# Kernel optimization log

Hardware: AMD Instinct MI355X
Metric: run time of the kernel (lower is better)

## Reference

```python
import jax, jax.numpy as jnp
import numpy as np

N = 50000   # nodes
E = 400000  # edges
G = 256     # graphs in batch
D = 256     # out_dim (scalar channel width)
VD = 16     # vector channel width after v_emb


def setup_inputs() -> dict:
    key = jax.random.key(0)
    ks = jax.random.split(key, 12)

    def rn(k, shape, scale=0.02):
        return (jax.random.normal(k, shape) * scale).astype(jnp.float32)

    return dict(
        node_s=jax.random.normal(ks[0], (N, 23), jnp.float32),
        node_v=jax.random.normal(ks[1], (N, 4, 3), jnp.float32),
        edge_s=jax.random.normal(ks[2], (E, 17), jnp.float32),
        edge_index=jax.random.randint(ks[3], (2, E), 0, N, jnp.int32),
        batch=jnp.sort(jax.random.randint(ks[4], (N,), 0, G, jnp.int32)),
        Ws=rn(ks[5], (23, D)), bs=jnp.zeros((D,), jnp.float32),
        Wv=rn(ks[6], (4, VD)), bv=jnp.zeros((VD,), jnp.float32),
        We=rn(ks[7], (18, D)), be=jnp.zeros((D,), jnp.float32),
        Wm1=rn(ks[8], (2 * D + VD + D, D)), bm1=jnp.zeros((D,), jnp.float32),
        Wm2=rn(ks[9], (D, D)), bm2=jnp.zeros((D,), jnp.float32),
        Wn=rn(ks[10], (D + VD, D)), bn=jnp.zeros((D,), jnp.float32),
        gamma=jnp.ones((D,), jnp.float32), beta=jnp.zeros((D,), jnp.float32),
    )


def reference(node_s, node_v, edge_s, edge_index, batch,
              Ws, bs, Wv, bv, We, be, Wm1, bm1, Wm2, bm2, Wn, bn, gamma, beta):
    # --- embeddings ---
    s = node_s @ Ws + bs                                            # [N, D]
    e_in = jnp.concatenate([edge_s, jnp.zeros((edge_s.shape[0], 1), edge_s.dtype)], axis=-1)  # no edge_v branch
    e = e_in @ We + be                                              # [E, D]
    # v_emb: Linear over the 4 vector channels -> [N, VD, 3]
    v = jnp.einsum('nkc,ko->noc', node_v, Wv) + bv[None, :, None]
    v_norm = jnp.linalg.norm(v, axis=-1)                            # [N, VD]

    # --- SimpleGVPConv: gather -> 2-layer MLP per edge -> scatter-mean ---
    src, dst = edge_index[0], edge_index[1]                         # PyG: s_j = s[src], s_i = s[dst]
    m_in = jnp.concatenate([s[dst], s[src], v_norm[src], e], axis=-1)  # [E, 2D+VD+D]
    m = jax.nn.relu(m_in @ Wm1 + bm1) @ Wm2 + bm2                   # [E, D]
    agg = jax.ops.segment_sum(m, dst, num_segments=N)               # [N, D]
    cnt = jax.ops.segment_sum(jnp.ones((E,), m.dtype), dst, num_segments=N)
    s = s + agg / jnp.maximum(cnt, 1.0)[:, None]                    # mean aggr + residual update

    # --- node MLP: Linear -> LayerNorm -> ReLU (dropout = eval identity) ---
    feat = jnp.concatenate([s, v_norm], axis=-1)                    # [N, D+VD]
    h = feat @ Wn + bn                                              # [N, D]
    mu = h.mean(axis=-1, keepdims=True)
    var = h.var(axis=-1, keepdims=True)
    h = (h - mu) * jax.lax.rsqrt(var + 1e-5) * gamma + beta
    h = jax.nn.relu(h)

    # --- global mean pool ---
    gsum = jax.ops.segment_sum(h, batch, num_segments=G)            # [G, D]
    gcnt = jax.ops.segment_sum(jnp.ones((h.shape[0],), h.dtype), batch, num_segments=G)
    return gsum / jnp.maximum(gcnt, 1.0)[:, None]
```

## Files before the change

### kernel.cpp

```cpp
#include <hip/hip_runtime.h>
#include <hip/hip_bf16.h>

typedef unsigned short u16;
typedef __attribute__((ext_vector_type(8))) short short8;
typedef __attribute__((ext_vector_type(4))) short short4v;
typedef __attribute__((ext_vector_type(4))) float f32x4;

#define NN 50000
#define EE 400000
#define GG 256
#define MP 50048
#define KS 64
#define K2 320

static __device__ __forceinline__ __hip_bfloat16 f2b(float x) { return __float2bfloat16(x); }
static __device__ __forceinline__ float u16tof(u16 v) {
    unsigned x = ((unsigned)v) << 16;
    float f;
    __builtin_memcpy(&f, &x, 4);
    return f;
}
static __device__ __forceinline__ u16 ftou16(float x) {
    __hip_bfloat16 h = __float2bfloat16(x);
    u16 b;
    __builtin_memcpy(&b, &h, 2);
    return b;
}
static __device__ __forceinline__ float rlf(float v, int l) {
    unsigned u;
    __builtin_memcpy(&u, &v, 4);
    unsigned r = (unsigned)__builtin_amdgcn_readlane((int)u, l);
    float f;
    __builtin_memcpy(&f, &r, 4);
    return f;
}

static __device__ __forceinline__ float dot256(const float* __restrict__ a,
                                               const float* __restrict__ b, int c) {
    const float* __restrict__ bp = b + c;
    float s0 = 0.f, s1 = 0.f, s2 = 0.f, s3 = 0.f;
    float s4 = 0.f, s5 = 0.f, s6 = 0.f, s7 = 0.f;
#pragma unroll 4
    for (int j = 0; j < 256; j += 8) {
        s0 += a[j]     * bp[(size_t)(j)     * 256];
        s1 += a[j + 1] * bp[(size_t)(j + 1) * 256];
        s2 += a[j + 2] * bp[(size_t)(j + 2) * 256];
        s3 += a[j + 3] * bp[(size_t)(j + 3) * 256];
        s4 += a[j + 4] * bp[(size_t)(j + 4) * 256];
        s5 += a[j + 5] * bp[(size_t)(j + 5) * 256];
        s6 += a[j + 6] * bp[(size_t)(j + 6) * 256];
        s7 += a[j + 7] * bp[(size_t)(j + 7) * 256];
    }
    return ((s0 + s1) + (s2 + s3)) + ((s4 + s5) + (s6 + s7));
}

__global__ __launch_bounds__(256) void phase1(const float* __restrict__ Wm1,
                                              const float* __restrict__ Wn,
                                              const float* __restrict__ Wm2,
                                              const float* __restrict__ We,
                                              const float* __restrict__ be,
                                              const float* __restrict__ bm1,
                                              const float* __restrict__ bm2,
                                              const float* __restrict__ Ws,
                                              const float* __restrict__ bs,
                                              __hip_bfloat16* __restrict__ W1pqT,
                                              __hip_bfloat16* __restrict__ W2T,
                                              float* __restrict__ Wc, float* __restrict__ bc,
                                              float* __restrict__ crow,
                                              const float* __restrict__ node_s,
                                              const float* __restrict__ node_v,
                                              const float* __restrict__ Wv,
                                              const float* __restrict__ bv,
                                              __hip_bfloat16* __restrict__ XL2,
                                              const int* __restrict__ ei,
                                              const int* __restrict__ batch,
                                              int* __restrict__ cnt,
                                              int* __restrict__ gstart) {
    int blk = blockIdx.x, tid = threadIdx.x;
    if (blk < 64) {
        int k = blk;
#pragma unroll
        for (int half = 0; half < 2; ++half) {
            int c = half * 256 + tid;
            int cc = c & 255;
            const float* Wm1h = (c < 256) ? Wm1 : (Wm1 + 256 * 256);
            float v = 0.f;
            if (k < 23) v = dot256(&Ws[k * 256], Wm1h, cc);
            else if (k < 39) { if (c >= 256) v = Wm1[(512 + (k - 23)) * 256 + cc]; }
            else if (k == 39) v = dot256(bs, Wm1h, cc);
            W1pqT[c * KS + k] = f2b(v);
        }
    } else if (blk < 384) {
        int k = blk - 64, c = tid;
        float v = 0.f;
        if (k < 23) v = dot256(&Ws[k * 256], Wn, c);
        else if (k < 39) v = Wn[(256 + (k - 23)) * 256 + c];
        else if (k == 39) v = dot256(bs, Wn, c);
        else if (k < 296) v = dot256(&Wm2[(k - 40) * 256], Wn, c);
        W2T[c * K2 + k] = f2b(v);
    } else if (blk < 403) {
        int b = blk - 384, c = tid;
        if (b < 17) Wc[b * 256 + c] = dot256(&We[b * 256], &Wm1[528 * 256], c);
        else if (b == 17) bc[c] = bm1[c] + dot256(be, &Wm1[528 * 256], c);
        else crow[c] = dot256(bm2, Wn, c);
    } else if (blk < 12903) {
        int w = tid >> 6, lane = tid & 63;
        int n = (blk - 403) * 4 + w;
        if (n < NN) {
            float lv = (lane < 23) ? node_s[(size_t)n * 23 + lane] : 0.f;
            float vv = (lane < 12) ? node_v[(size_t)n * 12 + lane] : 0.f;
            float nvk[12];
#pragma unroll
            for (int k = 0; k < 12; ++k) nvk[k] = __shfl(vv, k, 64);
            float vn = 0.f;
            if (lane < 16) {
                float b0 = bv[lane];
                float vx = b0, vy = b0, vz = b0;
#pragma unroll
                for (int k = 0; k < 4; ++k) {
                    float wv = Wv[k * 16 + lane];
                    vx += nvk[k * 3 + 0] * wv;
                    vy += nvk[k * 3 + 1] * wv;
                    vz += nvk[k * 3 + 2] * wv;
                }
                vn = sqrtf(vx * vx + vy * vy + vz * vz);
            }
            int vsrc = (lane >= 23 && lane < 39) ? (lane - 23) : 0;
            float vbc = __shfl(vn, vsrc, 64);
            float outv;
            if (lane < 23) outv = lv;
            else if (lane < 39) outv = vbc;
            else if (lane == 39) outv = 1.f;
            else outv = 0.f;
            __hip_bfloat16* row = XL2 + (size_t)n * K2;
            row[lane] = f2b(outv);
            if (lane < 24) row[296 + lane] = f2b(0.f);
        }
    } else if (blk < 14466) {
        int e = (blk - 12903) * 256 + tid;
        if (e < EE) atomicAdd(&cnt[ei[EE + e]], 1);
    } else {
        int n = (blk - 14466) * 256 + tid;
        if (n < NN) {
            int bn = batch[n];
            int bp = (n == 0) ? -1 : batch[n - 1];
            for (int g = bp + 1; g <= bn; ++g) gstart[g] = n;
            if (n == NN - 1)
                for (int g = bn + 1; g <= GG; ++g) gstart[g] = NN;
        }
    }
}

__global__ __launch_bounds__(256) void scan1(const int* __restrict__ cnt, int* __restrict__ rowptr,
                                             int* __restrict__ bsum) {
    int tid = threadIdx.x, i = blockIdx.x * 256 + tid;
    __shared__ int sd[256];
    int v = (i < NN) ? cnt[i] : 0;
    sd[tid] = v;
    __syncthreads();
    for (int off = 1; off < 256; off <<= 1) {
        int t = (tid >= off) ? sd[tid - off] : 0;
        __syncthreads();
        sd[tid] += t;
        __syncthreads();
    }
    if (i < NN) rowptr[i] = sd[tid] - v;
    if (tid == 255) bsum[blockIdx.x] = sd[255];
}
__global__ __launch_bounds__(256) void scan2(int* __restrict__ bsum, const int* __restrict__ gstart,
                                             float* __restrict__ ginv) {
    int c = threadIdx.x;
    __shared__ int sd[256];
    int v = (c < 196) ? bsum[c] : 0;
    sd[c] = v;
    __syncthreads();
    for (int off = 1; off < 256; off <<= 1) {
        int t = (c >= off) ? sd[c - off] : 0;
        __syncthreads();
        sd[c] += t;
        __syncthreads();
    }
    if (c < 196) bsum[c] = sd[c] - v;
    ginv[c] = 1.f / fmaxf((float)(gstart[c + 1] - gstart[c]), 1.f);
}
__global__ __launch_bounds__(256) void scan3(const int* __restrict__ cnt, const int* __restrict__ bsum,
                                             int* __restrict__ rowptr, int* __restrict__ cursor) {
    int i = blockIdx.x * 256 + threadIdx.x;
    if (i < NN) {
        int v = rowptr[i] + bsum[blockIdx.x];
        rowptr[i] = v;
        cursor[i] = v;
        if (i == NN - 1) rowptr[NN] = v + cnt[i];
    }
}

__global__ __launch_bounds__(256, 2) void gemm1_fill(const u16* __restrict__ A, const u16* __restrict__ Bt,
                                                     __hip_bfloat16* __restrict__ C,
                                                     const int* __restrict__ ei, int* __restrict__ cursor,
                                                     int* __restrict__ eid) {
    __shared__ __align__(16) u16 At[128 * 64];
    __shared__ __align__(16) u16 Bs[128 * 64];
    int blk = blockIdx.x, tid = threadIdx.x;
    if (blk >= 1564) {
        int e = (blk - 1564) * 256 + tid;
        if (e < EE) {
            int d = ei[EE + e];
            int pos = atomicAdd(&cursor[d], 1);
            eid[pos] = e;
        }
        return;
    }
    long m0 = (long)(blk >> 2) * 128;
    long n0 = (long)(blk & 3) * 128;
    int wid = tid >> 6, lane = tid & 63;
    int wm = wid >> 1, wn = wid & 1;
    int quad = lane >> 4, l16 = lane & 15;
    f32x4 acc[4][4] = {};
    int r0 = tid >> 3;
    int cc = (tid & 7) * 8;
    const u16* Ab = A + (m0 + r0) * K2 + cc;
    const u16* Bb = Bt + (n0 + r0) * KS + cc;
#pragma unroll
    for (int i = 0; i < 4; ++i) {
        int row = r0 + i * 32;
        __builtin_amdgcn_global_load_lds(
            (const __attribute__((address_space(1))) void*)(Ab + (long)(i * 32) * K2),
            (__attribute__((address_space(3))) void*)(&At[row * 64 + cc]), 16, 0, 0);
    }
#pragma unroll
    for (int i = 0; i < 4; ++i) {
        int row = r0 + i * 32;
        __builtin_amdgcn_global_load_lds(
            (const __attribute__((address_space(1))) void*)(Bb + (long)(i * 32) * KS),
            (__attribute__((address_space(3))) void*)(&Bs[row * 64 + cc]), 16, 0, 0);
    }
    __syncthreads();
#pragma unroll
    for (int kk = 0; kk < 64; kk += 32) {
        short8 af[4], bf[4];
#pragma unroll
        for (int mi = 0; mi < 4; ++mi)
            af[mi] = *(const short8*)&At[(wm * 64 + mi * 16 + l16) * 64 + kk + quad * 8];
#pragma unroll
        for (int ni = 0; ni < 4; ++ni)
            bf[ni] = *(const short8*)&Bs[(wn * 64 + ni * 16 + l16) * 64 + kk + quad * 8];
#pragma unroll
        for (int mi = 0; mi < 4; ++mi) {
#pragma unroll
            for (int ni = 0; ni < 4; ++ni)
                acc[mi][ni] = __builtin_amdgcn_mfma_f32_16x16x32_bf16(af[mi], bf[ni], acc[mi][ni], 0, 0, 0);
        }
    }
#pragma unroll
    for (int mi = 0; mi < 4; ++mi) {
#pragma unroll
        for (int ni = 0; ni < 4; ++ni) {
            long row = m0 + wm * 64 + mi * 16 + quad * 4;
            long col = n0 + wn * 64 + ni * 16 + l16;
#pragma unroll
            for (int r = 0; r < 4; ++r)
                C[(row + r) * 512 + col] = f2b(acc[mi][ni][r]);
        }
    }
}

__global__ __launch_bounds__(64, 1) void edge_agg(const u16* __restrict__ PQ,
                                                  const float* __restrict__ edge_s,
                                                  const int* __restrict__ ei, const int* __restrict__ eid,
                                                  const int* __restrict__ rowptr, const float* __restrict__ Wc,
                                                  const float* __restrict__ bc, __hip_bfloat16* __restrict__ XL2) {
    int lane = threadIdx.x;
    int n = blockIdx.x;
    int start = rowptr[n], deg = rowptr[n + 1] - start;
    f32x4 wc4[17];
#pragma unroll
    for (int k = 0; k < 17; ++k) wc4[k] = *(const f32x4*)&Wc[k * 256 + lane * 4];
    f32x4 bc4 = *(const f32x4*)&bc[lane * 4];
    short4v p4 = *(const short4v*)&PQ[(size_t)n * 512 + lane * 4];
    f32x4 pb;
#pragma unroll
    for (int i = 0; i < 4; ++i) pb[i] = u16tof((u16)p4[i]) + bc4[i];
    f32x4 acc = {0.f, 0.f, 0.f, 0.f};
    for (int base = 0; base < deg; base += 64) {
        int m = deg - base;
        if (m > 64) m = 64;
        int ee = 0, ss = 0;
        if (lane < m) {
            ee = eid[start + base + lane];
            ss = ei[ee];
        }
        int e0 = __builtin_amdgcn_readlane(ee, 0);
        int s0 = __builtin_amdgcn_readlane(ss, 0);
        short4v q0 = *(const short4v*)&PQ[(size_t)s0 * 512 + 256 + lane * 4];
        float es0 = (lane < 17) ? edge_s[(size_t)e0 * 17 + lane] : 0.f;
        for (int jj = 0; jj < m; ++jj) {
            short4v q1 = q0;
            float es1 = es0;
            if (jj + 1 < m) {
                int e1 = __builtin_amdgcn_readlane(ee, jj + 1);
                int s1 = __builtin_amdgcn_readlane(ss, jj + 1);
                q1 = *(const short4v*)&PQ[(size_t)s1 * 512 + 256 + lane * 4];
                es1 = (lane < 17) ? edge_s[(size_t)e1 * 17 + lane] : 0.f;
            }
            f32x4 ra = {0.f, 0.f, 0.f, 0.f};
            f32x4 rb = {0.f, 0.f, 0.f, 0.f};
#pragma unroll
            for (int k = 0; k < 8; ++k) ra += wc4[k] * rlf(es0, k);
#pragma unroll
            for (int k = 8; k < 17; ++k) rb += wc4[k] * rlf(es0, k);
#pragma unroll
            for (int i = 0; i < 4; ++i)
                acc[i] += fmaxf(pb[i] + u16tof((u16)q0[i]) + ra[i] + rb[i], 0.f);
            q0 = q1;
            es0 = es1;
        }
    }
    float inv = 1.f / fmaxf((float)deg, 1.f);
    short4v ov;
#pragma unroll
    for (int i = 0; i < 4; ++i) ov[i] = (short)ftou16(acc[i] * inv);
    *(short4v*)&XL2[(size_t)n * K2 + 40 + lane * 4] = ov;
}

__global__ __launch_bounds__(256, 2) void gemm2_lnp(const u16* __restrict__ A, const u16* __restrict__ Bt,
                                                    const int* __restrict__ cnt, const int* __restrict__ batch,
                                                    const float* __restrict__ bn, const float* __restrict__ crow,
                                                    const float* __restrict__ gamma, const float* __restrict__ beta,
                                                    const float* __restrict__ ginv, float* __restrict__ out) {
    __shared__ __align__(16) u16 At[64 * 64];
    __shared__ __align__(16) u16 Bs[256 * 64];
    __shared__ float rsum[4][64], rsum2[4][64];
    __shared__ int sdeg[64], sbatch[64];
    int tid = threadIdx.x;
    long m0 = (long)blockIdx.x * 64;
    int w = tid >> 6, lane = tid & 63;
    int quad = lane >> 4, l16 = lane & 15;
    f32x4 acc[4][4] = {};
    int r0 = tid >> 3;
    int cc = (tid & 7) * 8;
    const u16* Ab = A + (m0 + r0) * K2 + cc;
    const u16* Bb = Bt + (long)r0 * K2 + cc;
    for (int kt = 0; kt < K2; kt += 64) {
#pragma unroll
        for (int i = 0; i < 2; ++i) {
            int row = r0 + i * 32;
            __builtin_amdgcn_global_load_lds(
                (const __attribute__((address_space(1))) void*)(Ab + (long)(i * 32) * K2 + kt),
                (__attribute__((address_space(3))) void*)(&At[row * 64 + cc]), 16, 0, 0);
        }
#pragma unroll
        for (int i = 0; i < 8; ++i) {
            int row = r0 + i * 32;
            __builtin_amdgcn_global_load_lds(
                (const __attribute__((address_space(1))) void*)(Bb + (long)(i * 32) * K2 + kt),
                (__attribute__((address_space(3))) void*)(&Bs[row * 64 + cc]), 16, 0, 0);
        }
        __syncthreads();
#pragma unroll
        for (int kk = 0; kk < 64; kk += 32) {
            short8 af[4], bf[4];
#pragma unroll
            for (int mi = 0; mi < 4; ++mi)
                af[mi] = *(const short8*)&At[(mi * 16 + l16) * 64 + kk + quad * 8];
#pragma unroll
            for (int ni = 0; ni < 4; ++ni)
                bf[ni] = *(const short8*)&Bs[(w * 64 + ni * 16 + l16) * 64 + kk + quad * 8];
#pragma unroll
            for (int mi = 0; mi < 4; ++mi) {
#pragma unroll
                for (int ni = 0; ni < 4; ++ni)
                    acc[mi][ni] = __builtin_amdgcn_mfma_f32_16x16x32_bf16(af[mi], bf[ni], acc[mi][ni], 0, 0, 0);
            }
        }
        __syncthreads();
    }
    if (tid < 64) {
        long n = m0 + tid;
        sdeg[tid] = (n < NN) ? cnt[n] : 0;
        sbatch[tid] = (n < NN) ? batch[n] : -1;
    }
    __syncthreads();
    float bn_l[4], cr_l[4], g_l[4], be_l[4];
#pragma unroll
    for (int ni = 0; ni < 4; ++ni) {
        int col = w * 64 + ni * 16 + l16;
        bn_l[ni] = bn[col];
        cr_l[ni] = crow[col];
        g_l[ni] = gamma[col];
        be_l[ni] = beta[col];
    }
#pragma unroll
    for (int mi = 0; mi < 4; ++mi) {
#pragma unroll
        for (int r = 0; r < 4; ++r) {
            int row = mi * 16 + quad * 4 + r;
            float cr_on = (sdeg[row] > 0) ? 1.f : 0.f;
            float s = 0.f, s2 = 0.f;
#pragma unroll
            for (int ni = 0; ni < 4; ++ni) {
                float xv = acc[mi][ni][r] + bn_l[ni] + cr_on * cr_l[ni];
                acc[mi][ni][r] = xv;
                s += xv;
                s2 += xv * xv;
            }
            s += __shfl_xor(s, 1, 64);  s2 += __shfl_xor(s2, 1, 64);
            s += __shfl_xor(s, 2, 64);  s2 += __shfl_xor(s2, 2, 64);
            s += __shfl_xor(s, 4, 64);  s2 += __shfl_xor(s2, 4, 64);
            s += __shfl_xor(s, 8, 64);  s2 += __shfl_xor(s2, 8, 64);
            if (l16 == 0) { rsum[w][row] = s; rsum2[w][row] = s2; }
        }
    }
    __syncthreads();
    float mu_a[4][4], rs_a[4][4];
#pragma unroll
    for (int mi = 0; mi < 4; ++mi) {
#pragma unroll
        for (int r = 0; r < 4; ++r) {
            int row = mi * 16 + quad * 4 + r;
            float S = rsum[0][row] + rsum[1][row] + rsum[2][row] + rsum[3][row];
            float S2 = rsum2[0][row] + rsum2[1][row] + rsum2[2][row] + rsum2[3][row];
            float mu = S * (1.f / 256.f);
            mu_a[mi][r] = mu;
            rs_a[mi][r] = rsqrtf(S2 * (1.f / 256.f) - mu * mu + 1e-5f);
        }
    }
#pragma unroll
    for (int ni = 0; ni < 4; ++ni) {
        int col = w * 64 + ni * 16 + l16;
        float pacc = 0.f;
        int curg = -1;
#pragma unroll
        for (int mi = 0; mi < 4; ++mi) {
#pragma unroll
            for (int r = 0; r < 4; ++r) {
                int row = mi * 16 + quad * 4 + r;
                int g = sbatch[row];
                float y = (acc[mi][ni][r] - mu_a[mi][r]) * rs_a[mi][r] * g_l[ni] + be_l[ni];
                y = fmaxf(y, 0.f);
                if (g != curg) {
                    if (curg >= 0) atomicAdd(&out[curg * 256 + col], pacc * ginv[curg]);
                    pacc = 0.f;
                    curg = g;
                }
                if (g >= 0) pacc += y;
            }
        }
        if (curg >= 0) atomicAdd(&out[curg * 256 + col], pacc * ginv[curg]);
    }
}

extern "C" void kernel_launch(void* const* d_in, const int* in_sizes, int n_in,
                              void* d_out, int out_size, void* d_ws, size_t ws_size,
                              hipStream_t stream) {
    const float* node_s = (const float*)d_in[0];
    const float* node_v = (const float*)d_in[1];
    const float* edge_s = (const float*)d_in[2];
    const int* ei = (const int*)d_in[3];
    const int* batch = (const int*)d_in[4];
    const float* Ws = (const float*)d_in[5];
    const float* bs = (const float*)d_in[6];
    const float* Wv = (const float*)d_in[7];
    const float* bv = (const float*)d_in[8];
    const float* We = (const float*)d_in[9];
    const float* be = (const float*)d_in[10];
    const float* Wm1 = (const float*)d_in[11];
    const float* bm1 = (const float*)d_in[12];
    const float* Wm2 = (const float*)d_in[13];
    const float* bm2 = (const float*)d_in[14];
    const float* Wn = (const float*)d_in[15];
    const float* bn = (const float*)d_in[16];
    const float* gamma = (const float*)d_in[17];
    const float* beta = (const float*)d_in[18];

    char* ws = (char*)d_ws;
    size_t off = 0;
    auto take = [&](size_t n) {
        void* p = ws + off;
        off = (off + n + 255) & ~(size_t)255;
        return p;
    };
    __hip_bfloat16* XL2 = (__hip_bfloat16*)take((size_t)MP * K2 * 2);
    __hip_bfloat16* PQ = (__hip_bfloat16*)take((size_t)MP * 512 * 2);
    __hip_bfloat16* W1pqT = (__hip_bfloat16*)take(512 * KS * 2);
    __hip_bfloat16* W2T = (__hip_bfloat16*)take(256 * K2 * 2);
    float* Wc = (float*)take(17 * 256 * 4);
    float* bc = (float*)take(256 * 4);
    float* crow = (float*)take(256 * 4);
    int* cnt = (int*)take(NN * 4);
    int* gstart = (int*)take((GG + 1) * 4);
    float* ginv = (float*)take(GG * 4);
    int* rowptr = (int*)take((NN + 1) * 4);
    int* cursor = (int*)take(NN * 4);
    int* eid = (int*)take(EE * 4);
    int* bsum = (int*)take(256 * 4);

    hipMemsetAsync(cnt, 0, NN * 4, stream);
    hipMemsetAsync(d_out, 0, (size_t)out_size * 4, stream);

    phase1<<<14662, 256, 0, stream>>>(Wm1, Wn, Wm2, We, be, bm1, bm2, Ws, bs,
                                      W1pqT, W2T, Wc, bc, crow,
                                      node_s, node_v, Wv, bv, XL2, ei, batch, cnt, gstart);

    scan1<<<196, 256, 0, stream>>>(cnt, rowptr, bsum);
    scan2<<<1, 256, 0, stream>>>(bsum, gstart, ginv);
    scan3<<<196, 256, 0, stream>>>(cnt, bsum, rowptr, cursor);

    gemm1_fill<<<3127, 256, 0, stream>>>((const u16*)XL2, (const u16*)W1pqT, PQ, ei, cursor, eid);

    edge_agg<<<NN, 64, 0, stream>>>((const u16*)PQ, edge_s, ei, eid, rowptr, Wc, bc, XL2);

    gemm2_lnp<<<782, 256, 0, stream>>>((const u16*)XL2, (const u16*)W2T, cnt, batch,
                                       bn, crow, gamma, beta, ginv, (float*)d_out);
}
```

Measured before the change: 301.3 us.

## Compute per-edge edge-feature projection with MFMA in edge_agg

Replaces the per-edge scalar FMA loop (17 readlane broadcasts times 4 lanes) for edge_s·Wc with a bf16 MFMA over groups of 16 edges. The projected results are staged in LDS and then consumed in the gather loop. A packed bf16 copy of Wc is produced by an extra block in gemm1_fill. This cuts the ALU work per edge but adds LDS traffic and bf16 rounding of edge_s, Wc and the projected values. It also issues 16 MFMAs per group even when the group has fewer than 16 edges, and average degree is only about 8.

```diff
diff --git a/kernel.cpp b/kernel.cpp
--- a/kernel.cpp
+++ b/kernel.cpp
@@ -12,6 +12,7 @@
 #define MP 50048
 #define KS 64
 #define K2 320
+#define EWS 260
 
 static __device__ __forceinline__ __hip_bfloat16 f2b(float x) { return __float2bfloat16(x); }
 static __device__ __forceinline__ float u16tof(u16 v) {
@@ -25,14 +26,6 @@
     u16 b;
     __builtin_memcpy(&b, &h, 2);
     return b;
-}
-static __device__ __forceinline__ float rlf(float v, int l) {
-    unsigned u;
-    __builtin_memcpy(&u, &v, 4);
-    unsigned r = (unsigned)__builtin_amdgcn_readlane((int)u, l);
-    float f;
-    __builtin_memcpy(&f, &r, 4);
-    return f;
 }
 
 static __device__ __forceinline__ float dot256(const float* __restrict__ a,
@@ -197,11 +190,25 @@
 __global__ __launch_bounds__(256, 2) void gemm1_fill(const u16* __restrict__ A, const u16* __restrict__ Bt,
                                                      __hip_bfloat16* __restrict__ C,
                                                      const int* __restrict__ ei, int* __restrict__ cursor,
-                                                     int* __restrict__ eid) {
+                                                     int* __restrict__ eid,
+                                                     const float* __restrict__ Wc,
+                                                     u16* __restrict__ WcBf) {
     __shared__ __align__(16) u16 At[128 * 64];
     __shared__ __align__(16) u16 Bs[128 * 64];
     int blk = blockIdx.x, tid = threadIdx.x;
     if (blk >= 1564) {
+        if (blk == 3127) {
+            for (int idx = tid; idx < 8192; idx += 256) {
+                int ni = idx >> 9;
+                int l = (idx >> 3) & 63;
+                int j = idx & 7;
+                int k = ((l >> 4) << 3) + j;
+                int c = ni * 16 + (l & 15);
+                float v = (k < 17) ? Wc[k * 256 + c] : 0.f;
+                WcBf[idx] = ftou16(v);
+            }
+            return;
+        }
         int e = (blk - 1564) * 256 + tid;
         if (e < EE) {
             int d = ei[EE + e];
@@ -267,20 +274,25 @@
 __global__ __launch_bounds__(64, 1) void edge_agg(const u16* __restrict__ PQ,
                                                   const float* __restrict__ edge_s,
                                                   const int* __restrict__ ei, const int* __restrict__ eid,
-                                                  const int* __restrict__ rowptr, const float* __restrict__ Wc,
+                                                  const int* __restrict__ rowptr,
+                                                  const u16* __restrict__ WcBf,
                                                   const float* __restrict__ bc, __hip_bfloat16* __restrict__ XL2) {
+    __shared__ __align__(16) u16 EW[16 * EWS];
     int lane = threadIdx.x;
     int n = blockIdx.x;
     int start = rowptr[n], deg = rowptr[n + 1] - start;
-    f32x4 wc4[17];
-#pragma unroll
-    for (int k = 0; k < 17; ++k) wc4[k] = *(const f32x4*)&Wc[k * 256 + lane * 4];
+    int l16 = lane & 15, quad = lane >> 4;
+    short8 wcf[16];
+#pragma unroll
+    for (int ni = 0; ni < 16; ++ni)
+        wcf[ni] = *(const short8*)&WcBf[ni * 512 + lane * 8];
     f32x4 bc4 = *(const f32x4*)&bc[lane * 4];
     short4v p4 = *(const short4v*)&PQ[(size_t)n * 512 + lane * 4];
     f32x4 pb;
 #pragma unroll
     for (int i = 0; i < 4; ++i) pb[i] = u16tof((u16)p4[i]) + bc4[i];
     f32x4 acc = {0.f, 0.f, 0.f, 0.f};
+    const f32x4 zf = {0.f, 0.f, 0.f, 0.f};
     for (int base = 0; base < deg; base += 64) {
         int m = deg - base;
         if (m > 64) m = 64;
@@ -289,30 +301,46 @@
             ee = eid[start + base + lane];
             ss = ei[ee];
         }
-        int e0 = __builtin_amdgcn_readlane(ee, 0);
         int s0 = __builtin_amdgcn_readlane(ss, 0);
         short4v q0 = *(const short4v*)&PQ[(size_t)s0 * 512 + 256 + lane * 4];
-        float es0 = (lane < 17) ? edge_s[(size_t)e0 * 17 + lane] : 0.f;
-        for (int jj = 0; jj < m; ++jj) {
-            short4v q1 = q0;
-            float es1 = es0;
-            if (jj + 1 < m) {
-                int e1 = __builtin_amdgcn_readlane(ee, jj + 1);
-                int s1 = __builtin_amdgcn_readlane(ss, jj + 1);
-                q1 = *(const short4v*)&PQ[(size_t)s1 * 512 + 256 + lane * 4];
-                es1 = (lane < 17) ? edge_s[(size_t)e1 * 17 + lane] : 0.f;
-            }
-            f32x4 ra = {0.f, 0.f, 0.f, 0.f};
-            f32x4 rb = {0.f, 0.f, 0.f, 0.f};
-#pragma unroll
-            for (int k = 0; k < 8; ++k) ra += wc4[k] * rlf(es0, k);
-#pragma unroll
-            for (int k = 8; k < 17; ++k) rb += wc4[k] * rlf(es0, k);
-#pragma unroll
-            for (int i = 0; i < 4; ++i)
-                acc[i] += fmaxf(pb[i] + u16tof((u16)q0[i]) + ra[i] + rb[i], 0.f);
-            q0 = q1;
-            es0 = es1;
+        int ng = (m + 15) >> 4;
+        for (int g = 0; g < ng; ++g) {
+            int ev = __shfl(ee, g * 16 + l16, 64);
+            const float* ep = edge_s + (size_t)ev * 17 + quad * 8;
+            float a0 = 0.f, a1 = 0.f, a2 = 0.f, a3 = 0.f, a4 = 0.f, a5 = 0.f, a6 = 0.f, a7 = 0.f;
+            if (quad < 2) {
+                a0 = ep[0]; a1 = ep[1]; a2 = ep[2]; a3 = ep[3];
+                a4 = ep[4]; a5 = ep[5]; a6 = ep[6]; a7 = ep[7];
+            } else if (quad == 2) {
+                a0 = ep[0];
+            }
+            short8 af;
+            af[0] = (short)ftou16(a0); af[1] = (short)ftou16(a1);
+            af[2] = (short)ftou16(a2); af[3] = (short)ftou16(a3);
+            af[4] = (short)ftou16(a4); af[5] = (short)ftou16(a5);
+            af[6] = (short)ftou16(a6); af[7] = (short)ftou16(a7);
+#pragma unroll
+            for (int ni = 0; ni < 16; ++ni) {
+                f32x4 ew = __builtin_amdgcn_mfma_f32_16x16x32_bf16(af, wcf[ni], zf, 0, 0, 0);
+#pragma unroll
+                for (int r = 0; r < 4; ++r)
+                    EW[(quad * 4 + r) * EWS + ni * 16 + l16] = ftou16(ew[r]);
+            }
+            int mg = m - g * 16;
+            if (mg > 16) mg = 16;
+            for (int jj = 0; jj < mg; ++jj) {
+                int ja = g * 16 + jj;
+                short4v q1 = q0;
+                if (ja + 1 < m) {
+                    int s1 = __builtin_amdgcn_readlane(ss, ja + 1);
+                    q1 = *(const short4v*)&PQ[(size_t)s1 * 512 + 256 + lane * 4];
+                }
+                short4v ew4 = *(const short4v*)&EW[jj * EWS + lane * 4];
+#pragma unroll
+                for (int i = 0; i < 4; ++i)
+                    acc[i] += fmaxf(pb[i] + u16tof((u16)q0[i]) + u16tof((u16)ew4[i]), 0.f);
+                q0 = q1;
+            }
         }
     }
     float inv = 1.f / fmaxf((float)deg, 1.f);
@@ -486,6 +514,7 @@
     float* Wc = (float*)take(17 * 256 * 4);
     float* bc = (float*)take(256 * 4);
     float* crow = (float*)take(256 * 4);
+    u16* WcBf = (u16*)take(16 * 512 * 2);
     int* cnt = (int*)take(NN * 4);
     int* gstart = (int*)take((GG + 1) * 4);
     float* ginv = (float*)take(GG * 4);
@@ -505,9 +534,10 @@
     scan2<<<1, 256, 0, stream>>>(bsum, gstart, ginv);
     scan3<<<196, 256, 0, stream>>>(cnt, bsum, rowptr, cursor);
 
-    gemm1_fill<<<3127, 256, 0, stream>>>((const u16*)XL2, (const u16*)W1pqT, PQ, ei, cursor, eid);
-
-    edge_agg<<<NN, 64, 0, stream>>>((const u16*)PQ, edge_s, ei, eid, rowptr, Wc, bc, XL2);
+    gemm1_fill<<<3128, 256, 0, stream>>>((const u16*)XL2, (const u16*)W1pqT, PQ, ei, cursor, eid,
+                                         Wc, WcBf);
+
+    edge_agg<<<NN, 64, 0, stream>>>((const u16*)PQ, edge_s, ei, eid, rowptr, WcBf, bc, XL2);
 
     gemm2_lnp<<<782, 256, 0, stream>>>((const u16*)XL2, (const u16*)W2T, cnt, batch,
                                        bn, crow, gamma, beta, ginv, (float*)d_out);
```

New measurement: 311.9 us. 1.04x slower.
